# Performance work log

Hardware: AMD Instinct MI355X
Metric: run time of the kernel (lower is better)

Reference implementation:

```python
import jax, jax.numpy as jnp
import numpy as np

N = 5000        # nodes
F = 7699        # node feature dim (fixed by code)
E = 40000       # edges
ED = 3          # edge_dim (fixed by code)
H1, C1 = 4, 1024
H2, C2 = 1, 1024
NUM_OUT = 128
NEG_SLOPE = 0.2


def _glorot(key, shape):
    fan_in = shape[0]
    return jax.random.normal(key, shape, jnp.float32) / np.float32(np.sqrt(fan_in))


def setup_inputs() -> dict:
    key = jax.random.key(0)
    ks = jax.random.split(key, 16)
    x = jax.random.normal(ks[0], (N, F), jnp.float32)
    src = jax.random.randint(ks[1], (E,), 0, N)
    dst = jax.random.randint(ks[2], (E,), 0, N)
    src = jnp.where(src == dst, (src + 1) % N, src)  # no pre-existing self loops
    edge_index = jnp.stack([src, dst]).astype(jnp.int32)
    edge_attr = jax.random.normal(ks[3], (E, ED), jnp.float32)
    inp = {
        "x": x, "edge_index": edge_index, "edge_attr": edge_attr,
        # GATv2Conv #1: 7699 -> 1024, heads=4, edge_dim=3
        "W1l": _glorot(ks[4], (F, H1 * C1)), "b1l": jnp.zeros((H1 * C1,), jnp.float32),
        "W1r": _glorot(ks[5], (F, H1 * C1)), "b1r": jnp.zeros((H1 * C1,), jnp.float32),
        "W1e": _glorot(ks[6], (ED, H1 * C1)),
        "att1": _glorot(ks[7], (H1, C1)),
        "bias1": jnp.zeros((H1 * C1,), jnp.float32),
        # GATv2Conv #2: 4096 -> 1024, heads=1, edge_dim=3
        "W2l": _glorot(ks[8], (H1 * C1, H2 * C2)), "b2l": jnp.zeros((H2 * C2,), jnp.float32),
        "W2r": _glorot(ks[9], (H1 * C1, H2 * C2)), "b2r": jnp.zeros((H2 * C2,), jnp.float32),
        "W2e": _glorot(ks[10], (ED, H2 * C2)),
        "att2": _glorot(ks[11], (H2, C2)),
        "bias2": jnp.zeros((H2 * C2,), jnp.float32),
        # final Linear(1024, num_outputs)
        "Wlin": _glorot(ks[12], (C2, NUM_OUT)), "blin": jnp.zeros((NUM_OUT,), jnp.float32),
    }
    return inp


def gatv2_layer(x, src, dst, edge_attr, Wl, bl, Wr, br, We, att, bias, heads, out_ch):
    """PyG GATv2Conv with add_self_loops=True, fill_value='mean', concat=True."""
    n = x.shape[0]
    # self-loop edge_attr = mean of incoming edge attrs per node (fill_value='mean')
    deg = jax.ops.segment_sum(jnp.ones((src.shape[0],), jnp.float32), dst, num_segments=n)
    loop_attr = jax.ops.segment_sum(edge_attr, dst, num_segments=n) / jnp.maximum(deg, 1.0)[:, None]
    idx = jnp.arange(n, dtype=src.dtype)
    srcf = jnp.concatenate([src, idx])
    dstf = jnp.concatenate([dst, idx])
    ea = jnp.concatenate([edge_attr, loop_attr], axis=0)
    xl = (x @ Wl + bl).reshape(n, heads, out_ch)   # lin_l (source)
    xr = (x @ Wr + br).reshape(n, heads, out_ch)   # lin_r (target)
    ee = (ea @ We).reshape(-1, heads, out_ch)       # lin_edge (no bias)
    e = jax.nn.leaky_relu(xl[srcf] + xr[dstf] + ee, NEG_SLOPE)  # [E', H, C]
    logit = jnp.einsum('ehc,hc->eh', e, att)                     # [E', H]
    # segment softmax over destination nodes (every node has a self loop)
    m = jax.lax.stop_gradient(jax.ops.segment_max(logit, dstf, num_segments=n))
    a = jnp.exp(logit - m[dstf])
    denom = jax.ops.segment_sum(a, dstf, num_segments=n)
    alpha = a / (denom[dstf] + 1e-16)
    out = jax.ops.segment_sum(alpha[:, :, None] * xl[srcf], dstf, num_segments=n)  # [N,H,C]
    return out.reshape(n, heads * out_ch) + bias


def reference(x, edge_index, edge_attr,
              W1l, b1l, W1r, b1r, W1e, att1, bias1,
              W2l, b2l, W2r, b2r, W2e, att2, bias2,
              Wlin, blin):
    src, dst = edge_index[0], edge_index[1]
    h = gatv2_layer(x, src, dst, edge_attr, W1l, b1l, W1r, b1r, W1e, att1, bias1, H1, C1)
    h = gatv2_layer(h, src, dst, edge_attr, W2l, b2l, W2r, b2r, W2e, att2, bias2, H2, C2)
    return h @ Wlin + blin
```

## Files before the change

### kernel.cpp

```cpp
#include <hip/hip_runtime.h>
#include <cstdint>
#include <cstddef>

#define N_NODES 5000
#define F_IN    7699
#define KP1     7712
#define KT1     241
#define MP      5120
#define E_EDGES 40000
#define EFULL   45000
#define HC1     4096
#define N1      8192
#define HC2     1024
#define N2      2048
#define NOUT    128

typedef __bf16 bf16x8 __attribute__((ext_vector_type(8)));
typedef float  f32x4  __attribute__((ext_vector_type(4)));
typedef unsigned int u32x4 __attribute__((ext_vector_type(4)));
typedef unsigned short u16x8 __attribute__((ext_vector_type(8)));

using as1_uchar = unsigned char __attribute__((address_space(1)));
using as3_uchar = unsigned char __attribute__((address_space(3)));

__device__ __forceinline__ unsigned short f2bf(float f) {
  union { float f; unsigned int u; } v; v.f = f;
  return (unsigned short)((v.u + 0x7fffu + ((v.u >> 16) & 1u)) >> 16);
}
__device__ __forceinline__ float bf2f(unsigned short h) {
  union { unsigned int u; float f; } v; v.u = ((unsigned int)h) << 16;
  return v.f;
}

__device__ __forceinline__ void gload16(const void* g, void* l) {
  __builtin_amdgcn_global_load_lds(
      reinterpret_cast<const as1_uchar*>(reinterpret_cast<uintptr_t>(g)),
      reinterpret_cast<as3_uchar*>(reinterpret_cast<uintptr_t>(l)),
      16, 0, 0);
}



__global__ void k_split_x(const float* __restrict__ x, unsigned short* __restrict__ hi,
                          unsigned short* __restrict__ lo) {
  const int C8 = KP1 / 8;
  int ci = blockIdx.x * 256 + threadIdx.x;
  if (ci >= MP * C8) return;
  int r = ci / C8, c8 = ci % C8;
  int c = c8 * 8;
  u16x8 hb, lb;
  #pragma unroll
  for (int j = 0; j < 8; ++j) {
    float v = 0.f;
    if (r < N_NODES && (c + j) < F_IN) v = x[(size_t)r * F_IN + c + j];
    unsigned short h = f2bf(v);
    hb[j] = h; lb[j] = f2bf(v - bf2f(h));
  }
  size_t off = ((size_t)((r >> 7) * KT1 + (c >> 5)) * 4 + ((c >> 3) & 3)) * 1024 + (r & 127) * 8;
  *(u16x8*)&hi[off] = hb;
  *(u16x8*)&lo[off] = lb;
}


__global__ __launch_bounds__(256, 3) void k_gemm_bs(
    const unsigned short* __restrict__ Ahi, const unsigned short* __restrict__ Alo,
    const float* __restrict__ B0, const float* __restrict__ B1, int ldB, int halfNB,
    float* __restrict__ C, const float* __restrict__ bias0, const float* __restrict__ bias1,
    int halfN, int M, int ldC, int KT, int Klim, int gm)
{
  __shared__ __align__(16) unsigned short AhS[4096];
  __shared__ __align__(16) unsigned short AlS[4096];
  __shared__ __align__(16) unsigned short BhS[4096];
  __shared__ __align__(16) unsigned short BlS[4096];

  const int tid = threadIdx.x;
  const int lane = tid & 63;
  const int w = tid >> 6;
  const int wm = w >> 1, wn = w & 1;

  const int chunkg = gridDim.x >> 3;
  const int wg = (blockIdx.x & 7) * chunkg + (blockIdx.x >> 3);
  const int bm = wg % gm, bn = wg / gm;

  const float* Bp = (bn < halfNB) ? B0 : B1;
  const int cb = ((bn < halfNB) ? bn : bn - halfNB) * 128;

  f32x4 acc[4][4] = {};

  const unsigned short* AbH = Ahi + (size_t)bm * KT * 4096;
  const unsigned short* AbL = Alo + (size_t)bm * KT * 4096;
  const int sOff = w * 1024 + lane * 8;

  const int ccB = tid & 127;
  const int kB0 = (tid >> 7) * 16;
  const int c0  = (tid >> 7) * 2;

  const int fr = lane & 15;
  const int fchunk = (lane >> 4) * 1024;

  float breg[16];

  auto loadB = [&](int kt) {
    #pragma unroll
    for (int j = 0; j < 16; ++j) {
      int kg = kt * 32 + kB0 + j;
      breg[j] = (kg < Klim) ? Bp[(size_t)kg * ldB + cb + ccB] : 0.f;
    }
  };
  auto stageA = [&](int kt) {
    const unsigned short* bh = AbH + (size_t)kt * 4096 + sOff;
    const unsigned short* bl = AbL + (size_t)kt * 4096 + sOff;
    gload16(bh,       &AhS[w * 1024]);
    gload16(bh + 512, &AhS[w * 1024 + 512]);
    gload16(bl,       &AlS[w * 1024]);
    gload16(bl + 512, &AlS[w * 1024 + 512]);
  };
  auto convB = [&]() {
    #pragma unroll
    for (int u = 0; u < 2; ++u) {
      u32x4 hv, lv;
      #pragma unroll
      for (int m = 0; m < 4; ++m) {
        float a0f = breg[8 * u + 2 * m], a1f = breg[8 * u + 2 * m + 1];
        unsigned int ph, pl;
        asm("v_cvt_pk_bf16_f32 %0, %1, %2" : "=v"(ph) : "v"(a0f), "v"(a1f));
        union { unsigned int u_; float f; } h0, h1;
        h0.u_ = ph << 16; h1.u_ = ph & 0xFFFF0000u;
        float l0 = a0f - h0.f, l1 = a1f - h1.f;
        asm("v_cvt_pk_bf16_f32 %0, %1, %2" : "=v"(pl) : "v"(l0), "v"(l1));
        hv[m] = ph; lv[m] = pl;
      }
      const int off = (c0 + u) * 1024 + ccB * 8;
      *(u32x4*)&BhS[off] = hv;
      *(u32x4*)&BlS[off] = lv;
    }
  };

  loadB(0);
  stageA(0);
  convB();
  loadB(1);
  __syncthreads();

  for (int kt = 0; kt < KT; ++kt) {
    bf16x8 ah[4], al[4];
    #pragma unroll
    for (int i = 0; i < 4; ++i) {
      const int ro = fchunk + (wm * 64 + i * 16 + fr) * 8;
      ah[i] = *(const bf16x8*)&AhS[ro];
      al[i] = *(const bf16x8*)&AlS[ro];
    }
    #pragma unroll
    for (int j = 0; j < 4; ++j) {
      const int ro = fchunk + (wn * 64 + j * 16 + fr) * 8;
      bf16x8 bh = *(const bf16x8*)&BhS[ro];
      bf16x8 bl = *(const bf16x8*)&BlS[ro];
      #pragma unroll
      for (int i = 0; i < 4; ++i) {
        acc[i][j] = __builtin_amdgcn_mfma_f32_16x16x32_bf16(ah[i], bh, acc[i][j], 0, 0, 0);
        acc[i][j] = __builtin_amdgcn_mfma_f32_16x16x32_bf16(al[i], bh, acc[i][j], 0, 0, 0);
        acc[i][j] = __builtin_amdgcn_mfma_f32_16x16x32_bf16(ah[i], bl, acc[i][j], 0, 0, 0);
      }
    }
    if (kt + 1 < KT) {
      __syncthreads();
      stageA(kt + 1);
      convB();
      loadB(kt + 2);
      __syncthreads();
    }
  }

  const int rowb = bm * 128 + wm * 64 + (lane >> 4) * 4;
  const int colb = bn * 128 + wn * 64 + (lane & 15);
  #pragma unroll
  for (int i = 0; i < 4; ++i) {
    #pragma unroll
    for (int j = 0; j < 4; ++j) {
      int gc = colb + j * 16;
      float bvv = (gc < halfN) ? bias0[gc] : bias1[gc - halfN];
      #pragma unroll
      for (int r = 0; r < 4; ++r) {
        int gr = rowb + i * 16 + r;
        if (gr < M) C[(size_t)gr * ldC + gc] = acc[i][j][r] + bvv;
      }
    }
  }
}


__global__ void k_deg(const int* __restrict__ dst, const float* __restrict__ ea,
                      float* __restrict__ deg, float* __restrict__ lattr, int E) {
  int e = blockIdx.x * 256 + threadIdx.x;
  if (e >= E) return;
  int d = dst[e];
  atomicAdd(&deg[d], 1.f);
  atomicAdd(&lattr[d * 3 + 0], ea[e * 3 + 0]);
  atomicAdd(&lattr[d * 3 + 1], ea[e * 3 + 1]);
  atomicAdd(&lattr[d * 3 + 2], ea[e * 3 + 2]);
}

__global__ void k_lattr_fin(float* __restrict__ lattr, const float* __restrict__ deg, int n) {
  int i = blockIdx.x * 256 + threadIdx.x;
  if (i >= n) return;
  float dv = fmaxf(deg[i], 1.f);
  lattr[i * 3 + 0] /= dv; lattr[i * 3 + 1] /= dv; lattr[i * 3 + 2] /= dv;
}

__global__ void k_eafull(const float* __restrict__ ea, const float* __restrict__ lattr,
                         float* __restrict__ eaf, int E, int n) {
  int e = blockIdx.x * 256 + threadIdx.x;
  if (e >= E + n) return;
  const float* s = (e < E) ? &ea[(size_t)e * 3] : &lattr[(size_t)(e - E) * 3];
  eaf[e * 3 + 0] = s[0]; eaf[e * 3 + 1] = s[1]; eaf[e * 3 + 2] = s[2];
}

__global__ void k_count(const int* __restrict__ dst, int* __restrict__ cnt, int E, int n) {
  int e = blockIdx.x * 256 + threadIdx.x;
  if (e >= E + n) return;
  int d = (e < E) ? dst[e] : (e - E);
  atomicAdd(&cnt[d], 1);
}

__global__ void k_scan(const int* __restrict__ cnt, int* __restrict__ rowptr, int n) {
  int lane = threadIdx.x;
  int run = 0;
  for (int base = 0; base < n; base += 64) {
    int i = base + lane;
    int v = (i < n) ? cnt[i] : 0;
    #pragma unroll
    for (int off = 1; off < 64; off <<= 1) {
      int t = __shfl_up(v, off, 64);
      if (lane >= off) v += t;
    }
    if (i < n) rowptr[i + 1] = run + v;
    run += __shfl(v, 63, 64);
  }
  if (lane == 0) rowptr[0] = 0;
}

__global__ void k_fill(const int* __restrict__ dst, const int* __restrict__ rowptr,
                       int* __restrict__ fillc, int* __restrict__ elist, int E, int n) {
  int e = blockIdx.x * 256 + threadIdx.x;
  if (e >= E + n) return;
  int d = (e < E) ? dst[e] : (e - E);
  int pos = rowptr[d] + atomicAdd(&fillc[d], 1);
  elist[pos] = e;
}


template <int H, int ITERS>
__global__ __launch_bounds__(256) void k_logit(
    const float* __restrict__ xl, const float* __restrict__ xr, int strideX,
    const float* __restrict__ eaf, const float* __restrict__ We, const float* __restrict__ att,
    const int* __restrict__ src, const int* __restrict__ dst, int E,
    float* __restrict__ logit)
{
  const int e = blockIdx.x;
  const int tid = threadIdx.x;
  int s, d;
  if (e < E) { s = src[e]; d = dst[e]; } else { s = e - E; d = s; }
  const float ea0 = eaf[e * 3 + 0], ea1 = eaf[e * 3 + 1], ea2 = eaf[e * 3 + 2];
  constexpr int HC = ITERS * 256;
  const float* rl = xl + (size_t)s * strideX;
  const float* rr = xr + (size_t)d * strideX;
  float acc[H];
  #pragma unroll
  for (int h = 0; h < H; ++h) acc[h] = 0.f;
  #pragma unroll
  for (int i = 0; i < ITERS; ++i) {
    int hc = tid + (i << 8);
    float v = rl[hc] + rr[hc] + ea0 * We[hc] + ea1 * We[HC + hc] + ea2 * We[2 * HC + hc];
    v = (v > 0.f) ? v : 0.2f * v;
    acc[i >> 2] += v * att[hc];
  }
  __shared__ float red[H][4];
  const int lane = tid & 63, wv = tid >> 6;
  #pragma unroll
  for (int h = 0; h < H; ++h) {
    float v = acc[h];
    #pragma unroll
    for (int off = 32; off > 0; off >>= 1) v += __shfl_down(v, off, 64);
    if (lane == 0) red[h][wv] = v;
  }
  __syncthreads();
  if (tid < H)
    logit[(size_t)e * H + tid] = red[tid][0] + red[tid][1] + red[tid][2] + red[tid][3];
}

template <int H>
__global__ void k_stats(const float* __restrict__ logit, const int* __restrict__ rowptr,
                        const int* __restrict__ elist, float* __restrict__ mb, float* __restrict__ db)
{
  const int n = blockIdx.x;
  const int lane = threadIdx.x;
  const int start = rowptr[n], end = rowptr[n + 1];
  #pragma unroll
  for (int h = 0; h < H; ++h) {
    float m = -1e30f;
    for (int p = start + lane; p < end; p += 64)
      m = fmaxf(m, logit[(size_t)elist[p] * H + h]);
    #pragma unroll
    for (int off = 32; off > 0; off >>= 1) m = fmaxf(m, __shfl_down(m, off, 64));
    m = __shfl(m, 0, 64);
    float sum = 0.f;
    for (int p = start + lane; p < end; p += 64)
      sum += __expf(logit[(size_t)elist[p] * H + h] - m);
    #pragma unroll
    for (int off = 32; off > 0; off >>= 1) sum += __shfl_down(sum, off, 64);
    if (lane == 0) { mb[n * H + h] = m; db[n * H + h] = sum; }
  }
}

template <int H, int NC8, int KTo>
__global__ __launch_bounds__(256) void k_agg(
    const float* __restrict__ xl, int strideX,
    const int* __restrict__ rowptr, const int* __restrict__ elist, const int* __restrict__ src,
    const float* __restrict__ logit, const float* __restrict__ mb, const float* __restrict__ db,
    const float* __restrict__ bias,
    unsigned short* __restrict__ ohi, unsigned short* __restrict__ olo, int E)
{
  const int n = blockIdx.x;
  const int tid = threadIdx.x;
  constexpr int HC = H * 1024;
  float acc[NC8][8];
  #pragma unroll
  for (int q = 0; q < NC8; ++q)
    #pragma unroll
    for (int j = 0; j < 8; ++j) acc[q][j] = 0.f;
  const int start = rowptr[n], end = rowptr[n + 1];
  float mloc[H], dloc[H];
  #pragma unroll
  for (int h = 0; h < H; ++h) { mloc[h] = mb[n * H + h]; dloc[h] = db[n * H + h] + 1e-16f; }
  for (int p = start; p < end; ++p) {
    const int e = elist[p];
    const int s = (e < E) ? src[e] : (e - E);
    float al[H];
    #pragma unroll
    for (int h = 0; h < H; ++h)
      al[h] = __expf(logit[(size_t)e * H + h] - mloc[h]) / dloc[h];
    const float* row = xl + (size_t)s * strideX;
    #pragma unroll
    for (int q = 0; q < NC8; ++q) {
      const int c8 = tid + q * 256;
      if (c8 * 8 < HC) {
        float a = (H == 4) ? ((tid & 128) ? al[2 * q + 1] : al[2 * q]) : al[0];
        f32x4 v0 = *(const f32x4*)(row + c8 * 8);
        f32x4 v1 = *(const f32x4*)(row + c8 * 8 + 4);
        #pragma unroll
        for (int j = 0; j < 4; ++j) { acc[q][j] += a * v0[j]; acc[q][4 + j] += a * v1[j]; }
      }
    }
  }
  #pragma unroll
  for (int q = 0; q < NC8; ++q) {
    const int c8 = tid + q * 256;
    if (c8 * 8 < HC) {
      u16x8 hb, lb;
      #pragma unroll
      for (int j = 0; j < 8; ++j) {
        float v = acc[q][j] + bias[c8 * 8 + j];
        unsigned short h = f2bf(v);
        hb[j] = h; lb[j] = f2bf(v - bf2f(h));
      }
      size_t off = ((size_t)((n >> 7) * KTo + (c8 >> 2)) * 4 + (c8 & 3)) * 1024 + (n & 127) * 8;
      *(u16x8*)&ohi[off] = hb;
      *(u16x8*)&olo[off] = lb;
    }
  }
}


extern "C" void kernel_launch(void* const* d_in, const int* in_sizes, int n_in,
                              void* d_out, int out_size, void* d_ws, size_t ws_size,
                              hipStream_t stream) {
  const float* x    = (const float*)d_in[0];
  const int*   eidx = (const int*)d_in[1];
  const float* eattr= (const float*)d_in[2];
  const float* W1l  = (const float*)d_in[3];
  const float* b1l  = (const float*)d_in[4];
  const float* W1r  = (const float*)d_in[5];
  const float* b1r  = (const float*)d_in[6];
  const float* W1e  = (const float*)d_in[7];
  const float* att1 = (const float*)d_in[8];
  const float* bias1= (const float*)d_in[9];
  const float* W2l  = (const float*)d_in[10];
  const float* b2l  = (const float*)d_in[11];
  const float* W2r  = (const float*)d_in[12];
  const float* b2r  = (const float*)d_in[13];
  const float* W2e  = (const float*)d_in[14];
  const float* att2 = (const float*)d_in[15];
  const float* bias2= (const float*)d_in[16];
  const float* Wlin = (const float*)d_in[17];
  const float* blin = (const float*)d_in[18];
  float* out = (float*)d_out;

  char* ws = (char*)d_ws;
  const int* srcp = eidx;
  const int* dstp = eidx + E_EDGES;

  auto alignup = [](size_t v) { return (v + 255) & ~(size_t)255; };

  const size_t oXHI = 0;
  const size_t oXLO = oXHI + (size_t)MP * KP1 * 2;
  const size_t oXLR = oXLO + (size_t)MP * KP1 * 2;
  const size_t oS   = oXLR + (size_t)N_NODES * N1 * 4;
  const size_t oLATTR = alignup(oS);
  const size_t oDEG   = alignup(oLATTR + (size_t)N_NODES * 3 * 4);
  const size_t oEAF   = alignup(oDEG + (size_t)N_NODES * 4);
  const size_t oCNT   = alignup(oEAF + (size_t)EFULL * 3 * 4);
  const size_t oROW   = alignup(oCNT + (size_t)N_NODES * 4);
  const size_t oFILL  = alignup(oROW + (size_t)(N_NODES + 1) * 4);
  const size_t oELIST = alignup(oFILL + (size_t)N_NODES * 4);
  const size_t oLOGIT = alignup(oELIST + (size_t)EFULL * 4);
  const size_t oMB    = alignup(oLOGIT + (size_t)EFULL * 4 * 4);
  const size_t oDB    = alignup(oMB + (size_t)N_NODES * 4 * 4);
  const size_t oEND   = alignup(oDB + (size_t)N_NODES * 4 * 4);
  if (ws_size < oEND) return;

  const size_t oH1HI = oXHI;
  const size_t oH1LO = oXLO;
  const size_t oXLR2 = oXLR;
  const size_t oH2HI = oXLR + 64ull * 1024 * 1024;
  const size_t oH2LO = oXLR + 80ull * 1024 * 1024;

  unsigned short* XHI  = (unsigned short*)(ws + oXHI);
  unsigned short* XLO  = (unsigned short*)(ws + oXLO);
  float*          XLR  = (float*)(ws + oXLR);
  float*          LATTR= (float*)(ws + oLATTR);
  float*          DEG  = (float*)(ws + oDEG);
  float*          EAF  = (float*)(ws + oEAF);
  int*            CNT  = (int*)(ws + oCNT);
  int*            ROWP = (int*)(ws + oROW);
  int*            FILLC= (int*)(ws + oFILL);
  int*            ELIST= (int*)(ws + oELIST);
  float*          LOGIT= (float*)(ws + oLOGIT);
  float*          MB   = (float*)(ws + oMB);
  float*          DB   = (float*)(ws + oDB);
  unsigned short* H1HI = (unsigned short*)(ws + oH1HI);
  unsigned short* H1LO = (unsigned short*)(ws + oH1LO);
  float*          XLR2 = (float*)(ws + oXLR2);
  unsigned short* H2HI = (unsigned short*)(ws + oH2HI);
  unsigned short* H2LO = (unsigned short*)(ws + oH2LO);

  hipMemsetAsync(ws + oDEG,   0, (size_t)N_NODES * 4, stream);
  hipMemsetAsync(ws + oLATTR, 0, (size_t)N_NODES * 3 * 4, stream);
  hipMemsetAsync(ws + oCNT,   0, (size_t)N_NODES * 4, stream);
  hipMemsetAsync(ws + oFILL,  0, (size_t)N_NODES * 4, stream);

  const int gE  = (E_EDGES + 255) / 256;
  const int gEF = (EFULL + 255) / 256;
  const int gN  = (N_NODES + 255) / 256;

  k_deg<<<gE, 256, 0, stream>>>(dstp, eattr, DEG, LATTR, E_EDGES);
  k_lattr_fin<<<gN, 256, 0, stream>>>(LATTR, DEG, N_NODES);
  k_eafull<<<gEF, 256, 0, stream>>>(eattr, LATTR, EAF, E_EDGES, N_NODES);
  k_count<<<gEF, 256, 0, stream>>>(dstp, CNT, E_EDGES, N_NODES);
  k_scan<<<1, 64, 0, stream>>>(CNT, ROWP, N_NODES);
  k_fill<<<gEF, 256, 0, stream>>>(dstp, ROWP, FILLC, ELIST, E_EDGES, N_NODES);

  k_split_x<<<MP * (KP1 / 8) / 256, 256, 0, stream>>>(x, XHI, XLO);
  k_gemm_bs<<<64 * (MP / 128), 256, 0, stream>>>(
      XHI, XLO, W1l, W1r, HC1, 32,
      XLR, b1l, b1r, HC1, N_NODES, N1, KT1, F_IN, MP / 128);

  k_logit<4, 16><<<EFULL, 256, 0, stream>>>(XLR, XLR + HC1, N1, EAF, W1e, att1, srcp, dstp, E_EDGES, LOGIT);
  k_stats<4><<<N_NODES, 64, 0, stream>>>(LOGIT, ROWP, ELIST, MB, DB);
  hipMemsetAsync(ws + oH1HI, 0, (size_t)MP * HC1 * 2, stream);
  hipMemsetAsync(ws + oH1LO, 0, (size_t)MP * HC1 * 2, stream);
  k_agg<4, 2, HC1 / 32><<<N_NODES, 256, 0, stream>>>(
      XLR, N1, ROWP, ELIST, srcp, LOGIT, MB, DB, bias1, H1HI, H1LO, E_EDGES);

  k_gemm_bs<<<16 * (MP / 128), 256, 0, stream>>>(
      H1HI, H1LO, W2l, W2r, HC2, 8,
      XLR2, b2l, b2r, HC2, N_NODES, N2, HC1 / 32, HC1, MP / 128);

  k_logit<1, 4><<<EFULL, 256, 0, stream>>>(XLR2, XLR2 + HC2, N2, EAF, W2e, att2, srcp, dstp, E_EDGES, LOGIT);
  k_stats<1><<<N_NODES, 64, 0, stream>>>(LOGIT, ROWP, ELIST, MB, DB);
  hipMemsetAsync(ws + oH2HI, 0, (size_t)MP * HC2 * 2, stream);
  hipMemsetAsync(ws + oH2LO, 0, (size_t)MP * HC2 * 2, stream);
  k_agg<1, 1, HC2 / 32><<<N_NODES, 256, 0, stream>>>(
      XLR2, N2, ROWP, ELIST, srcp, LOGIT, MB, DB, bias2, H2HI, H2LO, E_EDGES);

  k_gemm_bs<<<1 * (MP / 128), 256, 0, stream>>>(
      H2HI, H2LO, Wlin, Wlin, NOUT, 1,
      out, blin, blin, NOUT, N_NODES, NOUT, HC2 / 32, HC2, MP / 128);
}
```

Measured before the change: 3.069 ms.

## Double-buffer LDS in split-bf16 GEMM and overlap staging with MFMA

The GEMM now keeps two LDS buffers per operand and stages the next k-tile's A (async loads) and converted B into the other buffer before computing on the current one. The two syncthreads per iteration become a single barrier with a partial vmcnt wait. The out-of-range B loads switch from a predicated zero to a load from a zeroed scratch buffer, which keeps the loads unconditional. MFMA sections run at raised wave priority, and launch bounds drop from 3 to 2 blocks per CU because LDS use doubles.

```diff
diff --git a/kernel.cpp b/kernel.cpp
--- a/kernel.cpp
+++ b/kernel.cpp
@@ -62,16 +62,16 @@
 }
 
 
-__global__ __launch_bounds__(256, 3) void k_gemm_bs(
+__global__ __launch_bounds__(256, 2) void k_gemm_bs(
     const unsigned short* __restrict__ Ahi, const unsigned short* __restrict__ Alo,
     const float* __restrict__ B0, const float* __restrict__ B1, int ldB, int halfNB,
     float* __restrict__ C, const float* __restrict__ bias0, const float* __restrict__ bias1,
-    int halfN, int M, int ldC, int KT, int Klim, int gm)
+    int halfN, int M, int ldC, int KT, int Klim, int gm, const float* __restrict__ zbuf)
 {
-  __shared__ __align__(16) unsigned short AhS[4096];
-  __shared__ __align__(16) unsigned short AlS[4096];
-  __shared__ __align__(16) unsigned short BhS[4096];
-  __shared__ __align__(16) unsigned short BlS[4096];
+  __shared__ __align__(16) unsigned short AhS[2 * 4096];
+  __shared__ __align__(16) unsigned short AlS[2 * 4096];
+  __shared__ __align__(16) unsigned short BhS[2 * 4096];
+  __shared__ __align__(16) unsigned short BlS[2 * 4096];
 
   const int tid = threadIdx.x;
   const int lane = tid & 63;
@@ -104,18 +104,19 @@
     #pragma unroll
     for (int j = 0; j < 16; ++j) {
       int kg = kt * 32 + kB0 + j;
-      breg[j] = (kg < Klim) ? Bp[(size_t)kg * ldB + cb + ccB] : 0.f;
+      const float* sp = (kg < Klim) ? (Bp + (size_t)kg * ldB + cb + ccB) : (zbuf + ccB);
+      breg[j] = *sp;
     }
   };
-  auto stageA = [&](int kt) {
+  auto stageA = [&](int kt, int p) {
     const unsigned short* bh = AbH + (size_t)kt * 4096 + sOff;
     const unsigned short* bl = AbL + (size_t)kt * 4096 + sOff;
-    gload16(bh,       &AhS[w * 1024]);
-    gload16(bh + 512, &AhS[w * 1024 + 512]);
-    gload16(bl,       &AlS[w * 1024]);
-    gload16(bl + 512, &AlS[w * 1024 + 512]);
+    gload16(bh,       &AhS[p * 4096 + w * 1024]);
+    gload16(bh + 512, &AhS[p * 4096 + w * 1024 + 512]);
+    gload16(bl,       &AlS[p * 4096 + w * 1024]);
+    gload16(bl + 512, &AlS[p * 4096 + w * 1024 + 512]);
   };
-  auto convB = [&]() {
+  auto convB = [&](int p) {
     #pragma unroll
     for (int u = 0; u < 2; ++u) {
       u32x4 hv, lv;
@@ -130,29 +131,38 @@
         asm("v_cvt_pk_bf16_f32 %0, %1, %2" : "=v"(pl) : "v"(l0), "v"(l1));
         hv[m] = ph; lv[m] = pl;
       }
-      const int off = (c0 + u) * 1024 + ccB * 8;
+      const int off = p * 4096 + (c0 + u) * 1024 + ccB * 8;
       *(u32x4*)&BhS[off] = hv;
       *(u32x4*)&BlS[off] = lv;
     }
   };
 
   loadB(0);
-  stageA(0);
-  convB();
+  stageA(0, 0);
+  convB(0);
   loadB(1);
-  __syncthreads();
-
+  asm volatile("s_waitcnt vmcnt(16) lgkmcnt(0)" ::: "memory");
+  __builtin_amdgcn_s_barrier();
+  __builtin_amdgcn_sched_barrier(0);
+
+  int p = 0;
   for (int kt = 0; kt < KT; ++kt) {
+    const int ktn = (kt + 1 < KT) ? kt + 1 : kt;
+    stageA(ktn, p ^ 1);
+    convB(p ^ 1);
+    loadB(kt + 2);
+
     bf16x8 ah[4], al[4];
     #pragma unroll
     for (int i = 0; i < 4; ++i) {
-      const int ro = fchunk + (wm * 64 + i * 16 + fr) * 8;
+      const int ro = p * 4096 + fchunk + (wm * 64 + i * 16 + fr) * 8;
       ah[i] = *(const bf16x8*)&AhS[ro];
       al[i] = *(const bf16x8*)&AlS[ro];
     }
+    __builtin_amdgcn_s_setprio(1);
     #pragma unroll
     for (int j = 0; j < 4; ++j) {
-      const int ro = fchunk + (wn * 64 + j * 16 + fr) * 8;
+      const int ro = p * 4096 + fchunk + (wn * 64 + j * 16 + fr) * 8;
       bf16x8 bh = *(const bf16x8*)&BhS[ro];
       bf16x8 bl = *(const bf16x8*)&BlS[ro];
       #pragma unroll
@@ -162,13 +172,12 @@
         acc[i][j] = __builtin_amdgcn_mfma_f32_16x16x32_bf16(ah[i], bl, acc[i][j], 0, 0, 0);
       }
     }
-    if (kt + 1 < KT) {
-      __syncthreads();
-      stageA(kt + 1);
-      convB();
-      loadB(kt + 2);
-      __syncthreads();
-    }
+    __builtin_amdgcn_s_setprio(0);
+
+    asm volatile("s_waitcnt vmcnt(16) lgkmcnt(0)" ::: "memory");
+    __builtin_amdgcn_s_barrier();
+    __builtin_amdgcn_sched_barrier(0);
+    p ^= 1;
   }
 
   const int rowb = bm * 128 + wm * 64 + (lane >> 4) * 4;
@@ -415,7 +424,8 @@
   const size_t oLOGIT = alignup(oELIST + (size_t)EFULL * 4);
   const size_t oMB    = alignup(oLOGIT + (size_t)EFULL * 4 * 4);
   const size_t oDB    = alignup(oMB + (size_t)N_NODES * 4 * 4);
-  const size_t oEND   = alignup(oDB + (size_t)N_NODES * 4 * 4);
+  const size_t oZBUF  = alignup(oDB + (size_t)N_NODES * 4 * 4);
+  const size_t oEND   = alignup(oZBUF + 512);
   if (ws_size < oEND) return;
 
   const size_t oH1HI = oXHI;
@@ -437,6 +447,7 @@
   float*          LOGIT= (float*)(ws + oLOGIT);
   float*          MB   = (float*)(ws + oMB);
   float*          DB   = (float*)(ws + oDB);
+  float*          ZBUF = (float*)(ws + oZBUF);
   unsigned short* H1HI = (unsigned short*)(ws + oH1HI);
   unsigned short* H1LO = (unsigned short*)(ws + oH1LO);
   float*          XLR2 = (float*)(ws + oXLR2);
@@ -447,6 +458,7 @@
   hipMemsetAsync(ws + oLATTR, 0, (size_t)N_NODES * 3 * 4, stream);
   hipMemsetAsync(ws + oCNT,   0, (size_t)N_NODES * 4, stream);
   hipMemsetAsync(ws + oFILL,  0, (size_t)N_NODES * 4, stream);
+  hipMemsetAsync(ws + oZBUF,  0, 512, stream);
 
   const int gE  = (E_EDGES + 255) / 256;
   const int gEF = (EFULL + 255) / 256;
@@ -462,7 +474,7 @@
   k_split_x<<<MP * (KP1 / 8) / 256, 256, 0, stream>>>(x, XHI, XLO);
   k_gemm_bs<<<64 * (MP / 128), 256, 0, stream>>>(
       XHI, XLO, W1l, W1r, HC1, 32,
-      XLR, b1l, b1r, HC1, N_NODES, N1, KT1, F_IN, MP / 128);
+      XLR, b1l, b1r, HC1, N_NODES, N1, KT1, F_IN, MP / 128, ZBUF);
 
   k_logit<4, 16><<<EFULL, 256, 0, stream>>>(XLR, XLR + HC1, N1, EAF, W1e, att1, srcp, dstp, E_EDGES, LOGIT);
   k_stats<4><<<N_NODES, 64, 0, stream>>>(LOGIT, ROWP, ELIST, MB, DB);
@@ -473,7 +485,7 @@
 
   k_gemm_bs<<<16 * (MP / 128), 256, 0, stream>>>(
       H1HI, H1LO, W2l, W2r, HC2, 8,
-      XLR2, b2l, b2r, HC2, N_NODES, N2, HC1 / 32, HC1, MP / 128);
+      XLR2, b2l, b2r, HC2, N_NODES, N2, HC1 / 32, HC1, MP / 128, ZBUF);
 
   k_logit<1, 4><<<EFULL, 256, 0, stream>>>(XLR2, XLR2 + HC2, N2, EAF, W2e, att2, srcp, dstp, E_EDGES, LOGIT);
   k_stats<1><<<N_NODES, 64, 0, stream>>>(LOGIT, ROWP, ELIST, MB, DB);
@@ -484,5 +496,5 @@
 
   k_gemm_bs<<<1 * (MP / 128), 256, 0, stream>>>(
       H2HI, H2LO, Wlin, Wlin, NOUT, 1,
-      out, blin, blin, NOUT, N_NODES, NOUT, HC2 / 32, HC2, MP / 128);
-}
+      out, blin, blin, NOUT, N_NODES, NOUT, HC2 / 32, HC2, MP / 128, ZBUF);
+}
```

Result: slower. 3.404 ms (+10.9%).

## Pre-split weights into bf16 tiles, use 32x32 MFMA, store projections as fp16

Applied to the files above, without the earlier changes.

Adds a kernel that converts each fp32 weight matrix once into tiled bf16 hi/lo pairs. The GEMM can then stage both operands through direct global-to-LDS loads instead of converting B in registers on every k-step. The GEMM switches from 16x16x32 to 32x32x16 MFMA tiles, raises wave priority around the MFMA block, and writes the layer projections as fp16. This halves traffic for the logit and aggregation gathers. In exchange it adds weight-split passes and extra workspace, splits layer 1 into two sequential GEMMs, and loses precision on the stored projections.

```diff
diff --git a/kernel.cpp b/kernel.cpp
--- a/kernel.cpp
+++ b/kernel.cpp
@@ -17,8 +17,10 @@
 
 typedef __bf16 bf16x8 __attribute__((ext_vector_type(8)));
 typedef float  f32x4  __attribute__((ext_vector_type(4)));
-typedef unsigned int u32x4 __attribute__((ext_vector_type(4)));
+typedef float  f32x16 __attribute__((ext_vector_type(16)));
 typedef unsigned short u16x8 __attribute__((ext_vector_type(8)));
+typedef _Float16 f16;
+typedef _Float16 f16x8 __attribute__((ext_vector_type(8)));
 
 using as1_uchar = unsigned char __attribute__((address_space(1)));
 using as3_uchar = unsigned char __attribute__((address_space(3)));
@@ -62,11 +64,42 @@
 }
 
 
-__global__ __launch_bounds__(256, 3) void k_gemm_bs(
+__global__ void k_split_w(const float* __restrict__ W,
+                          unsigned short* __restrict__ hi, unsigned short* __restrict__ lo,
+                          int K, int Nsrc, int c0, int KT, int rowOffset) {
+  __shared__ float tile[32][33];
+  const int tid = threadIdx.x;
+  const int kt = blockIdx.x;
+  const int n0 = blockIdx.y * 32;
+  #pragma unroll
+  for (int i = tid >> 5; i < 32; i += 8) {
+    int k = kt * 32 + i;
+    tile[i][tid & 31] = (k < K) ? W[(size_t)k * Nsrc + c0 + n0 + (tid & 31)] : 0.f;
+  }
+  __syncthreads();
+  if (tid < 128) {
+    const int nn = tid >> 2, kc = (tid & 3) << 3;
+    const int n = rowOffset + n0 + nn;
+    u16x8 hb, lb;
+    #pragma unroll
+    for (int j = 0; j < 8; ++j) {
+      float v = tile[kc + j][nn];
+      unsigned short h = f2bf(v);
+      hb[j] = h; lb[j] = f2bf(v - bf2f(h));
+    }
+    size_t off = ((size_t)((n >> 7) * KT + kt) * 4 + (kc >> 3)) * 1024 + (n & 127) * 8;
+    *(u16x8*)&hi[off] = hb;
+    *(u16x8*)&lo[off] = lb;
+  }
+}
+
+
+template <int OF16>
+__global__ __launch_bounds__(256, 3) void k_gemm_bb(
     const unsigned short* __restrict__ Ahi, const unsigned short* __restrict__ Alo,
-    const float* __restrict__ B0, const float* __restrict__ B1, int ldB, int halfNB,
-    float* __restrict__ C, const float* __restrict__ bias0, const float* __restrict__ bias1,
-    int halfN, int M, int ldC, int KT, int Klim, int gm)
+    const unsigned short* __restrict__ Bhi, const unsigned short* __restrict__ Blo,
+    void* __restrict__ Cp, const float* __restrict__ bias0, const float* __restrict__ bias1,
+    int halfN, int M, int ldC, int KT, int gm)
 {
   __shared__ __align__(16) unsigned short AhS[4096];
   __shared__ __align__(16) unsigned short AlS[4096];
@@ -82,107 +115,77 @@
   const int wg = (blockIdx.x & 7) * chunkg + (blockIdx.x >> 3);
   const int bm = wg % gm, bn = wg / gm;
 
-  const float* Bp = (bn < halfNB) ? B0 : B1;
-  const int cb = ((bn < halfNB) ? bn : bn - halfNB) * 128;
-
-  f32x4 acc[4][4] = {};
+  f32x16 acc[2][2] = {};
 
   const unsigned short* AbH = Ahi + (size_t)bm * KT * 4096;
   const unsigned short* AbL = Alo + (size_t)bm * KT * 4096;
+  const unsigned short* BbH = Bhi + (size_t)bn * KT * 4096;
+  const unsigned short* BbL = Blo + (size_t)bn * KT * 4096;
   const int sOff = w * 1024 + lane * 8;
 
-  const int ccB = tid & 127;
-  const int kB0 = (tid >> 7) * 16;
-  const int c0  = (tid >> 7) * 2;
-
-  const int fr = lane & 15;
-  const int fchunk = (lane >> 4) * 1024;
-
-  float breg[16];
-
-  auto loadB = [&](int kt) {
-    #pragma unroll
-    for (int j = 0; j < 16; ++j) {
-      int kg = kt * 32 + kB0 + j;
-      breg[j] = (kg < Klim) ? Bp[(size_t)kg * ldB + cb + ccB] : 0.f;
-    }
+  const int r5 = lane & 31, h5 = lane >> 5;
+
+  auto stage = [&](int kt) {
+    const size_t o = (size_t)kt * 4096 + sOff;
+    gload16(AbH + o,       &AhS[w * 1024]);
+    gload16(AbH + o + 512, &AhS[w * 1024 + 512]);
+    gload16(AbL + o,       &AlS[w * 1024]);
+    gload16(AbL + o + 512, &AlS[w * 1024 + 512]);
+    gload16(BbH + o,       &BhS[w * 1024]);
+    gload16(BbH + o + 512, &BhS[w * 1024 + 512]);
+    gload16(BbL + o,       &BlS[w * 1024]);
+    gload16(BbL + o + 512, &BlS[w * 1024 + 512]);
   };
-  auto stageA = [&](int kt) {
-    const unsigned short* bh = AbH + (size_t)kt * 4096 + sOff;
-    const unsigned short* bl = AbL + (size_t)kt * 4096 + sOff;
-    gload16(bh,       &AhS[w * 1024]);
-    gload16(bh + 512, &AhS[w * 1024 + 512]);
-    gload16(bl,       &AlS[w * 1024]);
-    gload16(bl + 512, &AlS[w * 1024 + 512]);
-  };
-  auto convB = [&]() {
-    #pragma unroll
-    for (int u = 0; u < 2; ++u) {
-      u32x4 hv, lv;
+
+  stage(0);
+  __syncthreads();
+
+  for (int kt = 0; kt < KT; ++kt) {
+    bf16x8 ah[2][2], al[2][2];
+    #pragma unroll
+    for (int i = 0; i < 2; ++i)
       #pragma unroll
-      for (int m = 0; m < 4; ++m) {
-        float a0f = breg[8 * u + 2 * m], a1f = breg[8 * u + 2 * m + 1];
-        unsigned int ph, pl;
-        asm("v_cvt_pk_bf16_f32 %0, %1, %2" : "=v"(ph) : "v"(a0f), "v"(a1f));
-        union { unsigned int u_; float f; } h0, h1;
-        h0.u_ = ph << 16; h1.u_ = ph & 0xFFFF0000u;
-        float l0 = a0f - h0.f, l1 = a1f - h1.f;
-        asm("v_cvt_pk_bf16_f32 %0, %1, %2" : "=v"(pl) : "v"(l0), "v"(l1));
-        hv[m] = ph; lv[m] = pl;
+      for (int kh = 0; kh < 2; ++kh) {
+        const int ro = (kh * 2 + h5) * 1024 + (wm * 64 + i * 32 + r5) * 8;
+        ah[i][kh] = *(const bf16x8*)&AhS[ro];
+        al[i][kh] = *(const bf16x8*)&AlS[ro];
       }
-      const int off = (c0 + u) * 1024 + ccB * 8;
-      *(u32x4*)&BhS[off] = hv;
-      *(u32x4*)&BlS[off] = lv;
-    }
-  };
-
-  loadB(0);
-  stageA(0);
-  convB();
-  loadB(1);
-  __syncthreads();
-
-  for (int kt = 0; kt < KT; ++kt) {
-    bf16x8 ah[4], al[4];
-    #pragma unroll
-    for (int i = 0; i < 4; ++i) {
-      const int ro = fchunk + (wm * 64 + i * 16 + fr) * 8;
-      ah[i] = *(const bf16x8*)&AhS[ro];
-      al[i] = *(const bf16x8*)&AlS[ro];
-    }
-    #pragma unroll
-    for (int j = 0; j < 4; ++j) {
-      const int ro = fchunk + (wn * 64 + j * 16 + fr) * 8;
-      bf16x8 bh = *(const bf16x8*)&BhS[ro];
-      bf16x8 bl = *(const bf16x8*)&BlS[ro];
+    __builtin_amdgcn_s_setprio(1);
+    #pragma unroll
+    for (int j = 0; j < 2; ++j) {
       #pragma unroll
-      for (int i = 0; i < 4; ++i) {
-        acc[i][j] = __builtin_amdgcn_mfma_f32_16x16x32_bf16(ah[i], bh, acc[i][j], 0, 0, 0);
-        acc[i][j] = __builtin_amdgcn_mfma_f32_16x16x32_bf16(al[i], bh, acc[i][j], 0, 0, 0);
-        acc[i][j] = __builtin_amdgcn_mfma_f32_16x16x32_bf16(ah[i], bl, acc[i][j], 0, 0, 0);
+      for (int kh = 0; kh < 2; ++kh) {
+        const int ro = (kh * 2 + h5) * 1024 + (wn * 64 + j * 32 + r5) * 8;
+        bf16x8 bh = *(const bf16x8*)&BhS[ro];
+        bf16x8 bl = *(const bf16x8*)&BlS[ro];
+        #pragma unroll
+        for (int i = 0; i < 2; ++i) {
+          acc[i][j] = __builtin_amdgcn_mfma_f32_32x32x16_bf16(ah[i][kh], bh, acc[i][j], 0, 0, 0);
+          acc[i][j] = __builtin_amdgcn_mfma_f32_32x32x16_bf16(al[i][kh], bh, acc[i][j], 0, 0, 0);
+          acc[i][j] = __builtin_amdgcn_mfma_f32_32x32x16_bf16(ah[i][kh], bl, acc[i][j], 0, 0, 0);
+        }
       }
     }
-    if (kt + 1 < KT) {
-      __syncthreads();
-      stageA(kt + 1);
-      convB();
-      loadB(kt + 2);
-      __syncthreads();
-    }
-  }
-
-  const int rowb = bm * 128 + wm * 64 + (lane >> 4) * 4;
-  const int colb = bn * 128 + wn * 64 + (lane & 15);
-  #pragma unroll
-  for (int i = 0; i < 4; ++i) {
-    #pragma unroll
-    for (int j = 0; j < 4; ++j) {
-      int gc = colb + j * 16;
-      float bvv = (gc < halfN) ? bias0[gc] : bias1[gc - halfN];
+    __builtin_amdgcn_s_setprio(0);
+    __syncthreads();
+    if (kt + 1 < KT) stage(kt + 1);
+    __syncthreads();
+  }
+
+  #pragma unroll
+  for (int i = 0; i < 2; ++i) {
+    #pragma unroll
+    for (int j = 0; j < 2; ++j) {
+      const int gc = bn * 128 + wn * 64 + j * 32 + r5;
+      const float bv = (gc < halfN) ? bias0[gc] : bias1[gc - halfN];
       #pragma unroll
-      for (int r = 0; r < 4; ++r) {
-        int gr = rowb + i * 16 + r;
-        if (gr < M) C[(size_t)gr * ldC + gc] = acc[i][j][r] + bvv;
+      for (int reg = 0; reg < 16; ++reg) {
+        const int gr = bm * 128 + wm * 64 + i * 32 + (reg & 3) + 8 * (reg >> 2) + 4 * h5;
+        if (gr < M) {
+          float v = acc[i][j][reg] + bv;
+          if (OF16) ((f16*)Cp)[(size_t)gr * ldC + gc] = (f16)v;
+          else      ((float*)Cp)[(size_t)gr * ldC + gc] = v;
+        }
       }
     }
   }
@@ -251,7 +254,7 @@
 
 template <int H, int ITERS>
 __global__ __launch_bounds__(256) void k_logit(
-    const float* __restrict__ xl, const float* __restrict__ xr, int strideX,
+    const f16* __restrict__ xl, const f16* __restrict__ xr, int strideX,
     const float* __restrict__ eaf, const float* __restrict__ We, const float* __restrict__ att,
     const int* __restrict__ src, const int* __restrict__ dst, int E,
     float* __restrict__ logit)
@@ -262,15 +265,16 @@
   if (e < E) { s = src[e]; d = dst[e]; } else { s = e - E; d = s; }
   const float ea0 = eaf[e * 3 + 0], ea1 = eaf[e * 3 + 1], ea2 = eaf[e * 3 + 2];
   constexpr int HC = ITERS * 256;
-  const float* rl = xl + (size_t)s * strideX;
-  const float* rr = xr + (size_t)d * strideX;
+  const f16* rl = xl + (size_t)s * strideX;
+  const f16* rr = xr + (size_t)d * strideX;
   float acc[H];
   #pragma unroll
   for (int h = 0; h < H; ++h) acc[h] = 0.f;
   #pragma unroll
   for (int i = 0; i < ITERS; ++i) {
     int hc = tid + (i << 8);
-    float v = rl[hc] + rr[hc] + ea0 * We[hc] + ea1 * We[HC + hc] + ea2 * We[2 * HC + hc];
+    float v = (float)rl[hc] + (float)rr[hc]
+            + ea0 * We[hc] + ea1 * We[HC + hc] + ea2 * We[2 * HC + hc];
     v = (v > 0.f) ? v : 0.2f * v;
     acc[i >> 2] += v * att[hc];
   }
@@ -314,7 +318,7 @@
 
 template <int H, int NC8, int KTo>
 __global__ __launch_bounds__(256) void k_agg(
-    const float* __restrict__ xl, int strideX,
+    const f16* __restrict__ xl, int strideX,
     const int* __restrict__ rowptr, const int* __restrict__ elist, const int* __restrict__ src,
     const float* __restrict__ logit, const float* __restrict__ mb, const float* __restrict__ db,
     const float* __restrict__ bias,
@@ -339,16 +343,15 @@
     #pragma unroll
     for (int h = 0; h < H; ++h)
       al[h] = __expf(logit[(size_t)e * H + h] - mloc[h]) / dloc[h];
-    const float* row = xl + (size_t)s * strideX;
+    const f16* row = xl + (size_t)s * strideX;
     #pragma unroll
     for (int q = 0; q < NC8; ++q) {
       const int c8 = tid + q * 256;
       if (c8 * 8 < HC) {
         float a = (H == 4) ? ((tid & 128) ? al[2 * q + 1] : al[2 * q]) : al[0];
-        f32x4 v0 = *(const f32x4*)(row + c8 * 8);
-        f32x4 v1 = *(const f32x4*)(row + c8 * 8 + 4);
+        f16x8 v = *(const f16x8*)(row + c8 * 8);
         #pragma unroll
-        for (int j = 0; j < 4; ++j) { acc[q][j] += a * v0[j]; acc[q][4 + j] += a * v1[j]; }
+        for (int j = 0; j < 8; ++j) acc[q][j] += a * (float)v[j];
       }
     }
   }
@@ -404,7 +407,9 @@
   const size_t oXHI = 0;
   const size_t oXLO = oXHI + (size_t)MP * KP1 * 2;
   const size_t oXLR = oXLO + (size_t)MP * KP1 * 2;
-  const size_t oS   = oXLR + (size_t)N_NODES * N1 * 4;
+  const size_t oBH  = oXLR + (size_t)N_NODES * N1 * 2;
+  const size_t oBL  = oBH + (size_t)4096 * KP1 * 2;
+  const size_t oS   = oBL + (size_t)4096 * KP1 * 2;
   const size_t oLATTR = alignup(oS);
   const size_t oDEG   = alignup(oLATTR + (size_t)N_NODES * 3 * 4);
   const size_t oEAF   = alignup(oDEG + (size_t)N_NODES * 4);
@@ -421,12 +426,18 @@
   const size_t oH1HI = oXHI;
   const size_t oH1LO = oXLO;
   const size_t oXLR2 = oXLR;
-  const size_t oH2HI = oXLR + 64ull * 1024 * 1024;
-  const size_t oH2LO = oXLR + 80ull * 1024 * 1024;
+  const size_t oH2HI = oXLR + 32ull * 1024 * 1024;
+  const size_t oH2LO = oXLR + 48ull * 1024 * 1024;
+  const size_t oB2H  = oBH;
+  const size_t oB2L  = oBL;
+  const size_t oB3H  = oBH;
+  const size_t oB3L  = oBH + 1ull * 1024 * 1024;
 
   unsigned short* XHI  = (unsigned short*)(ws + oXHI);
   unsigned short* XLO  = (unsigned short*)(ws + oXLO);
-  float*          XLR  = (float*)(ws + oXLR);
+  f16*            XLR  = (f16*)(ws + oXLR);
+  unsigned short* BH   = (unsigned short*)(ws + oBH);
+  unsigned short* BL   = (unsigned short*)(ws + oBL);
   float*          LATTR= (float*)(ws + oLATTR);
   float*          DEG  = (float*)(ws + oDEG);
   float*          EAF  = (float*)(ws + oEAF);
@@ -439,9 +450,13 @@
   float*          DB   = (float*)(ws + oDB);
   unsigned short* H1HI = (unsigned short*)(ws + oH1HI);
   unsigned short* H1LO = (unsigned short*)(ws + oH1LO);
-  float*          XLR2 = (float*)(ws + oXLR2);
+  f16*            XLR2 = (f16*)(ws + oXLR2);
   unsigned short* H2HI = (unsigned short*)(ws + oH2HI);
   unsigned short* H2LO = (unsigned short*)(ws + oH2LO);
+  unsigned short* B2H  = (unsigned short*)(ws + oB2H);
+  unsigned short* B2L  = (unsigned short*)(ws + oB2L);
+  unsigned short* B3H  = (unsigned short*)(ws + oB3H);
+  unsigned short* B3L  = (unsigned short*)(ws + oB3L);
 
   hipMemsetAsync(ws + oDEG,   0, (size_t)N_NODES * 4, stream);
   hipMemsetAsync(ws + oLATTR, 0, (size_t)N_NODES * 3 * 4, stream);
@@ -460,9 +475,14 @@
   k_fill<<<gEF, 256, 0, stream>>>(dstp, ROWP, FILLC, ELIST, E_EDGES, N_NODES);
 
   k_split_x<<<MP * (KP1 / 8) / 256, 256, 0, stream>>>(x, XHI, XLO);
-  k_gemm_bs<<<64 * (MP / 128), 256, 0, stream>>>(
-      XHI, XLO, W1l, W1r, HC1, 32,
-      XLR, b1l, b1r, HC1, N_NODES, N1, KT1, F_IN, MP / 128);
+
+  k_split_w<<<dim3(KT1, HC1 / 32), 256, 0, stream>>>(W1l, BH, BL, F_IN, HC1, 0, KT1, 0);
+  k_gemm_bb<1><<<(HC1 / 128) * (MP / 128), 256, 0, stream>>>(
+      XHI, XLO, BH, BL, XLR, b1l, b1l, HC1, N_NODES, N1, KT1, MP / 128);
+
+  k_split_w<<<dim3(KT1, HC1 / 32), 256, 0, stream>>>(W1r, BH, BL, F_IN, HC1, 0, KT1, 0);
+  k_gemm_bb<1><<<(HC1 / 128) * (MP / 128), 256, 0, stream>>>(
+      XHI, XLO, BH, BL, XLR + HC1, b1r, b1r, HC1, N_NODES, N1, KT1, MP / 128);
 
   k_logit<4, 16><<<EFULL, 256, 0, stream>>>(XLR, XLR + HC1, N1, EAF, W1e, att1, srcp, dstp, E_EDGES, LOGIT);
   k_stats<4><<<N_NODES, 64, 0, stream>>>(LOGIT, ROWP, ELIST, MB, DB);
@@ -471,9 +491,10 @@
   k_agg<4, 2, HC1 / 32><<<N_NODES, 256, 0, stream>>>(
       XLR, N1, ROWP, ELIST, srcp, LOGIT, MB, DB, bias1, H1HI, H1LO, E_EDGES);
 
-  k_gemm_bs<<<16 * (MP / 128), 256, 0, stream>>>(
-      H1HI, H1LO, W2l, W2r, HC2, 8,
-      XLR2, b2l, b2r, HC2, N_NODES, N2, HC1 / 32, HC1, MP / 128);
+  k_split_w<<<dim3(HC1 / 32, HC2 / 32), 256, 0, stream>>>(W2l, B2H, B2L, HC1, HC2, 0, HC1 / 32, 0);
+  k_split_w<<<dim3(HC1 / 32, HC2 / 32), 256, 0, stream>>>(W2r, B2H, B2L, HC1, HC2, 0, HC1 / 32, HC2);
+  k_gemm_bb<1><<<(N2 / 128) * (MP / 128), 256, 0, stream>>>(
+      H1HI, H1LO, B2H, B2L, XLR2, b2l, b2r, HC2, N_NODES, N2, HC1 / 32, MP / 128);
 
   k_logit<1, 4><<<EFULL, 256, 0, stream>>>(XLR2, XLR2 + HC2, N2, EAF, W2e, att2, srcp, dstp, E_EDGES, LOGIT);
   k_stats<1><<<N_NODES, 64, 0, stream>>>(LOGIT, ROWP, ELIST, MB, DB);
@@ -482,7 +503,7 @@
   k_agg<1, 1, HC2 / 32><<<N_NODES, 256, 0, stream>>>(
       XLR2, N2, ROWP, ELIST, srcp, LOGIT, MB, DB, bias2, H2HI, H2LO, E_EDGES);
 
-  k_gemm_bs<<<1 * (MP / 128), 256, 0, stream>>>(
-      H2HI, H2LO, Wlin, Wlin, NOUT, 1,
-      out, blin, blin, NOUT, N_NODES, NOUT, HC2 / 32, HC2, MP / 128);
-}
+  k_split_w<<<dim3(HC2 / 32, NOUT / 32), 256, 0, stream>>>(Wlin, B3H, B3L, HC2, NOUT, 0, HC2 / 32, 0);
+  k_gemm_bb<0><<<(NOUT / 128) * (MP / 128), 256, 0, stream>>>(
+      H2HI, H2LO, B3H, B3L, out, blin, blin, NOUT, N_NODES, NOUT, HC2 / 32, MP / 128);
+}
```

New measurement: 2.997 ms. 2.3% less time.
